# Optimization experiments

Measured on AMD Instinct MI355X. Metric: run time of the kernel, lower is better.

The kernel has to match this reference:

```python
import jax, jax.numpy as jnp
import numpy as np

N = 50000      # nodes
E = 800000     # edges (before self-loops)
G = 64         # graphs in batch
IN, HID, OUT, H = 128, 64, 64, 4
NEG_SLOPE = 0.2
BN_EPS = 1e-5


def setup_inputs() -> dict:
    key = jax.random.key(0)
    ks = jax.random.split(key, 16)
    s = 0.1
    return {
        "x": jax.random.normal(ks[0], (N, IN), jnp.float32),
        "edge_index": jax.random.randint(ks[1], (2, E), 0, N, dtype=jnp.int64),
        "batch": jnp.sort(jax.random.randint(ks[2], (N,), 0, G, dtype=jnp.int64)),
        "num_graphs": G,
        "W1": jax.random.normal(ks[3], (IN, H * HID), jnp.float32) * s,
        "att_src1": jax.random.normal(ks[4], (H, HID), jnp.float32) * s,
        "att_dst1": jax.random.normal(ks[5], (H, HID), jnp.float32) * s,
        "b1": jnp.zeros((HID,), jnp.float32),
        "W2": jax.random.normal(ks[6], (HID, H * OUT), jnp.float32) * s,
        "att_src2": jax.random.normal(ks[7], (H, OUT), jnp.float32) * s,
        "att_dst2": jax.random.normal(ks[8], (H, OUT), jnp.float32) * s,
        "b2": jnp.zeros((OUT,), jnp.float32),
        "gate_w1": jax.random.normal(ks[9], (OUT, OUT), jnp.float32) * s,
        "gate_b1": jnp.zeros((OUT,), jnp.float32),
        "bn_gamma": jnp.ones((OUT,), jnp.float32),
        "bn_beta": jnp.zeros((OUT,), jnp.float32),
        "gate_w2": jax.random.normal(ks[10], (OUT, 1), jnp.float32) * s,
        "gate_b2": jnp.zeros((1,), jnp.float32),
        "lin_w": jax.random.normal(ks[11], (OUT, 1), jnp.float32) * s,
        "lin_b": jnp.zeros((1,), jnp.float32),
    }


def segment_softmax(e, seg, num_segments):
    # numerically stable softmax over segments (per-destination / per-graph)
    m = jax.ops.segment_max(e, seg, num_segments=num_segments)
    m = jnp.where(jnp.isfinite(m), m, 0.0)
    ex = jnp.exp(e - m[seg])
    den = jax.ops.segment_sum(ex, seg, num_segments=num_segments)
    return ex / (den[seg] + 1e-16)


def gat_conv(x, src, dst, n, W, a_src, a_dst, b, heads, ch):
    h = (x @ W).reshape(n, heads, ch)                 # [N,H,C]
    asrc = jnp.sum(h * a_src, axis=-1)                # [N,H]
    adst = jnp.sum(h * a_dst, axis=-1)                # [N,H]
    e = jax.nn.leaky_relu(asrc[src] + adst[dst], NEG_SLOPE)   # [E',H]
    alpha = segment_softmax(e, dst, n)                # softmax over incoming edges
    out = jax.ops.segment_sum(h[src] * alpha[:, :, None], dst, num_segments=n)
    return jnp.mean(out, axis=1) + b                  # concat=False -> head mean


def reference(x, edge_index, batch, num_graphs, W1, att_src1, att_dst1, b1,
              W2, att_src2, att_dst2, b2, gate_w1, gate_b1, bn_gamma, bn_beta,
              gate_w2, gate_b2, lin_w, lin_b):
    n = x.shape[0]
    loop = jnp.arange(n, dtype=edge_index.dtype)      # PyG add_self_loops default
    src = jnp.concatenate([edge_index[0], loop])
    dst = jnp.concatenate([edge_index[1], loop])

    out = jax.nn.sigmoid(gat_conv(x, src, dst, n, W1, att_src1, att_dst1, b1, H, HID))
    out = jax.nn.sigmoid(gat_conv(out, src, dst, n, W2, att_src2, att_dst2, b2, H, OUT))

    # GlobalAttention pooling; gate_nn = Linear -> BN(eval, rm=0, rv=1) -> ReLU -> Linear
    g = out @ gate_w1 + gate_b1
    g = (g / jnp.sqrt(1.0 + BN_EPS)) * bn_gamma + bn_beta
    g = jax.nn.relu(g) @ gate_w2 + gate_b2            # [N,1]
    gate = segment_softmax(g, batch, num_graphs)      # per-graph softmax
    pooled = jax.ops.segment_sum(gate * out, batch, num_segments=num_graphs)  # [G,OUT]

    return jax.nn.sigmoid(pooled @ lin_w + lin_b)     # [G,1]
```

## Files before the change

kernel.cpp:

```cpp
#include <hip/hip_runtime.h>


constexpr int NN = 50000;
constexpr int EE = 800000;
constexpr int NG = 64;
constexpr float NEG = 0.2f;
constexpr int MT = NN / 16;
constexpr int SLOTS = 64;
constexpr int CH = 16;
constexpr int GB = (MT + 3) / 4;

constexpr int EB_EDGES = 4096;
constexpr int EBN = (EE + EB_EDGES - 1) / EB_EDGES;
constexpr int NBKT = (NN + 255) / 256;
constexpr int CAP = 48;
constexpr int OVFCAP = 8192;

static_assert(NN % 4 == 0, "aggregate barrier assumes no early-exit waves");

using bf16x8 = __attribute__((ext_vector_type(8))) __bf16;
using f32x4  = __attribute__((ext_vector_type(4))) float;
using f32x2  = __attribute__((ext_vector_type(2))) float;

__device__ __forceinline__ float wred(float v) {
#pragma unroll
  for (int o = 32; o; o >>= 1) v += __shfl_down(v, o);
  return v;
}
__device__ __forceinline__ float sigmoidf(float v) { return 1.f / (1.f + __expf(-v)); }
__device__ __forceinline__ float lrelu(float v) { return fmaxf(v, NEG * v); }
__device__ __forceinline__ unsigned short f2b(float f) {
  union { float f; unsigned u; } v; v.f = f;
  unsigned r = v.u + 0x7fff + ((v.u >> 16) & 1);
  return (unsigned short)(r >> 16);
}
__device__ __forceinline__ float b2f(unsigned short b) {
  union { unsigned u; float f; } v; v.u = ((unsigned)b) << 16;
  return v.f;
}

__global__ void prep_kernel(const float* __restrict__ W1, const float* __restrict__ W2,
                            const float* __restrict__ gw1, const float* __restrict__ gamma,
                            const int* __restrict__ batch,
                            unsigned short* __restrict__ W1b, unsigned short* __restrict__ W2b,
                            unsigned short* __restrict__ Bg, int* __restrict__ goffs,
                            int* __restrict__ ovf_cnt) {
  int b = blockIdx.x;
  if (b < 128) {
    int idx = b * 256 + threadIdx.x;
    int j = idx & 7, lane = (idx >> 3) & 63, rest = idx >> 9;
    int kc = rest & 3, ntile = rest >> 2;
    W1b[idx] = f2b(W1[(kc * 32 + (lane >> 4) * 8 + j) * 256 + ntile * 16 + (lane & 15)]);
    return;
  }
  if (b < 192) {
    int idx = (b - 128) * 256 + threadIdx.x;
    int j = idx & 7, lane = (idx >> 3) & 63, rest = idx >> 9;
    int kc = rest & 1, ntile = rest >> 1;
    W2b[idx] = f2b(W2[(kc * 32 + (lane >> 4) * 8 + j) * 256 + ntile * 16 + (lane & 15)]);
    return;
  }
  if (b < 208) {
    int idx = (b - 192) * 256 + threadIdx.x;
    int j = idx & 7, lane = (idx >> 3) & 63, rest = idx >> 9;
    int kc = rest & 1, nt = rest >> 1;
    int k = kc * 32 + (lane >> 4) * 8 + j;
    int n = nt * 16 + (lane & 15);
    Bg[idx] = f2b(gw1[k * 64 + n] * gamma[n] * rsqrtf(1.f + 1e-5f));
    return;
  }
  if (threadIdx.x == 0) *ovf_cnt = 0;
  int g = threadIdx.x;
  if (g <= NG) {
    int lo = 0, hi = NN;
    while (lo < hi) {
      int mid = (lo + hi) >> 1;
      if (batch[mid] < g) lo = mid + 1; else hi = mid;
    }
    goffs[g] = lo;
  }
}

template <int KC>
__device__ __forceinline__ void gemm_body(int mt, int lane, const bf16x8* av,
                                          const unsigned short* Bp,
                                          unsigned char* __restrict__ C8,
                                          const float* __restrict__ att_s,
                                          const float* __restrict__ att_d,
                                          float* __restrict__ asrc,
                                          float* __restrict__ adst) {
  int m0 = mt * 16;
  int q = lane >> 4, r = lane & 15;
  f32x4 acc[16] = {};
#pragma unroll
  for (int kc = 0; kc < KC; ++kc) {
#pragma unroll
    for (int nt = 0; nt < 16; ++nt) {
      bf16x8 b = *(const bf16x8*)&Bp[(((unsigned)nt * KC + kc) * 64 + lane) * 8];
      acc[nt] = __builtin_amdgcn_mfma_f32_16x16x32_bf16(av[kc], b, acc[nt], 0, 0, 0);
    }
  }
#pragma unroll
  for (int reg = 0; reg < 4; ++reg) {
    unsigned row = m0 + q * 4 + reg;
    uint4 pk;
    int w;
    w = __builtin_amdgcn_cvt_pk_fp8_f32(acc[0][reg], acc[1][reg], 0, false);
    w = __builtin_amdgcn_cvt_pk_fp8_f32(acc[2][reg], acc[3][reg], w, true);
    pk.x = (unsigned)w;
    w = __builtin_amdgcn_cvt_pk_fp8_f32(acc[4][reg], acc[5][reg], 0, false);
    w = __builtin_amdgcn_cvt_pk_fp8_f32(acc[6][reg], acc[7][reg], w, true);
    pk.y = (unsigned)w;
    w = __builtin_amdgcn_cvt_pk_fp8_f32(acc[8][reg], acc[9][reg], 0, false);
    w = __builtin_amdgcn_cvt_pk_fp8_f32(acc[10][reg], acc[11][reg], w, true);
    pk.z = (unsigned)w;
    w = __builtin_amdgcn_cvt_pk_fp8_f32(acc[12][reg], acc[13][reg], 0, false);
    w = __builtin_amdgcn_cvt_pk_fp8_f32(acc[14][reg], acc[15][reg], w, true);
    pk.w = (unsigned)w;
    *(uint4*)(C8 + (size_t)row * 256 + (unsigned)r * 16) = pk;
  }
  float ps[4][4] = {}, pd[4][4] = {};
#pragma unroll
  for (int head = 0; head < 4; ++head) {
#pragma unroll
    for (int i = 0; i < 4; ++i) {
      float sv = att_s[head * 64 + i * 16 + r];
      float dv = att_d[head * 64 + i * 16 + r];
#pragma unroll
      for (int reg = 0; reg < 4; ++reg) {
        ps[head][reg] += acc[head * 4 + i][reg] * sv;
        pd[head][reg] += acc[head * 4 + i][reg] * dv;
      }
    }
  }
#pragma unroll
  for (int head = 0; head < 4; ++head)
#pragma unroll
    for (int reg = 0; reg < 4; ++reg)
#pragma unroll
      for (int o = 1; o < 16; o <<= 1) {
        ps[head][reg] += __shfl_xor(ps[head][reg], o);
        pd[head][reg] += __shfl_xor(pd[head][reg], o);
      }
  if (r == 0) {
#pragma unroll
    for (int reg = 0; reg < 4; ++reg) {
      int row = m0 + q * 4 + reg;
#pragma unroll
      for (int head = 0; head < 4; ++head) {
        asrc[row * 4 + head] = ps[head][reg];
        adst[row * 4 + head] = pd[head][reg];
      }
    }
  }
}

__global__ void gemm1_build_kernel(const float* __restrict__ x,
                                   const unsigned short* __restrict__ W1b,
                                   unsigned char* __restrict__ C8,
                                   const float* __restrict__ att_s,
                                   const float* __restrict__ att_d,
                                   float* __restrict__ asrc, float* __restrict__ adst,
                                   const int* __restrict__ ei,
                                   unsigned* __restrict__ bins,
                                   int* __restrict__ binCnt,
                                   int* __restrict__ ovf_cnt,
                                   unsigned* __restrict__ ovf) {
  __shared__ union {
    unsigned short B[128 * 256];
    int hist[NBKT];
  } smem;
  int b = blockIdx.x;
  if (b < GB) {
    int wave = threadIdx.x >> 6, lane = threadIdx.x & 63;
    int mt0 = b * 4 + wave;
    int mt = min(mt0, MT - 1);
    int q = lane >> 4, r = lane & 15;
#pragma unroll
    for (int it = 0; it < 16; ++it)
      ((uint4*)smem.B)[it * 256 + threadIdx.x] = ((const uint4*)W1b)[it * 256 + threadIdx.x];
    bf16x8 av[4];
    {
      const float* Arow = x + (size_t)(mt * 16 + r) * 128 + q * 8;
      float4 f0[4], f1[4];
#pragma unroll
      for (int kc = 0; kc < 4; ++kc) {
        f0[kc] = *(const float4*)(Arow + kc * 32);
        f1[kc] = *(const float4*)(Arow + kc * 32 + 4);
      }
#pragma unroll
      for (int kc = 0; kc < 4; ++kc) {
        union { bf16x8 v; unsigned short s[8]; } u;
        u.s[0] = f2b(f0[kc].x); u.s[1] = f2b(f0[kc].y);
        u.s[2] = f2b(f0[kc].z); u.s[3] = f2b(f0[kc].w);
        u.s[4] = f2b(f1[kc].x); u.s[5] = f2b(f1[kc].y);
        u.s[6] = f2b(f1[kc].z); u.s[7] = f2b(f1[kc].w);
        av[kc] = u.v;
      }
    }
    __syncthreads();
    if (mt0 >= MT) return;
    gemm_body<4>(mt, lane, av, smem.B, C8, att_s, att_d, asrc, adst);
    return;
  }
  int hb = b - GB;
  for (int t = threadIdx.x; t < NBKT; t += 256) smem.hist[t] = 0;
  __syncthreads();
  int e0 = hb * EB_EDGES + threadIdx.x * 16;
#pragma unroll
  for (int k4 = 0; k4 < 4; ++k4) {
    int e = e0 + k4 * 4;
    if (e >= EE) break;
    int4 s4 = *(const int4*)&ei[e];
    int4 d4 = *(const int4*)&ei[EE + e];
    int ss[4] = {s4.x, s4.y, s4.z, s4.w};
    int dd[4] = {d4.x, d4.y, d4.z, d4.w};
#pragma unroll
    for (int u = 0; u < 4; ++u) {
      if (e + u >= EE) break;
      int src = ss[u], dst = dd[u];
      int bkt = dst >> 8;
      int rr = atomicAdd(&smem.hist[bkt], 1);
      if (rr < CAP) {
        bins[((unsigned)hb * NBKT + bkt) * CAP + rr] =
            (unsigned)src | ((unsigned)(dst & 255) << 16);
      } else {
        int o = atomicAdd(ovf_cnt, 1);
        if (o < OVFCAP) ovf[o] = (unsigned)src | ((unsigned)dst << 16);
      }
    }
  }
  __syncthreads();
  for (int t = threadIdx.x; t < NBKT; t += 256) binCnt[hb * NBKT + t] = smem.hist[t];
}

__global__ __launch_bounds__(1024) void csr_build_kernel(
    const unsigned* __restrict__ bins, const int* __restrict__ binCnt,
    const int* __restrict__ ovf_cnt, const unsigned* __restrict__ ovf,
    unsigned short* __restrict__ csr16, int* __restrict__ cnt) {
  int b = blockIdx.x;
  __shared__ int hist[256];
  int t = threadIdx.x;
  int node0 = b << 8;
  if (t < 256) {
    hist[t] = 1;
    int node = node0 + t;
    if (node < NN) csr16[(unsigned)node * SLOTS] = (unsigned short)node;
  }
  __syncthreads();
  int wave = t >> 6, lane = t & 63;
  for (int i = wave; i < EBN; i += 16) {
    int c = binCnt[i * NBKT + b];
    if (c > CAP) c = CAP;
    for (int base = 0; base < c; base += 64) {
      int j = base + lane;
      if (j < c) {
        unsigned p = bins[((unsigned)i * NBKT + b) * CAP + j];
        int dl = p >> 16, src = p & 0xffff;
        int r = atomicAdd(&hist[dl], 1);
        if (r < SLOTS) csr16[(unsigned)(node0 + dl) * SLOTS + r] = (unsigned short)src;
      }
    }
  }
  __syncthreads();
  int oc = *ovf_cnt;
  if (oc > OVFCAP) oc = OVFCAP;
  for (int j = t; j < oc; j += 1024) {
    unsigned p = ovf[j];
    int dst = (int)(p >> 16);
    if ((dst >> 8) == b) {
      int r = atomicAdd(&hist[dst & 255], 1);
      if (r < SLOTS) csr16[(unsigned)dst * SLOTS + r] = (unsigned short)(p & 0xffff);
    }
  }
  __syncthreads();
  if (t < 256) {
    int node = node0 + t;
    if (node < NN) cnt[node] = hist[t];
  }
}

__global__ void aggregate_kernel(const unsigned char* __restrict__ h8,
                                 const float* __restrict__ asrc,
                                 const float* __restrict__ adst,
                                 const int* __restrict__ cnt,
                                 const unsigned short* __restrict__ csr_src,
                                 const float* __restrict__ bias,
                                 unsigned short* __restrict__ outb) {
  int wave = threadIdx.x >> 6, lane = threadIdx.x & 63;
  int node = blockIdx.x * 4 + wave;
  int deg = min(cnt[node], SLOTS);
  int hgrp = lane >> 4;
  int q4 = lane >> 4;
  int r16 = lane & 15;
  float adh = adst[node * 4 + hgrp];
  int src_all = csr_src[(unsigned)node * SLOTS + lane];
  __shared__ float wtab[4][256];
  float* wlds = wtab[wave];
  float den = 0.f;
#pragma unroll
  for (int i = 0; i < 4; ++i) {
    int slot = i * 16 + r16;
    float w = 0.f;
    if (i * 16 < deg) {
      int s = __shfl(src_all, slot);
      bool valid = slot < deg;
      float xv = asrc[(unsigned)(valid ? s : 0) * 4 + hgrp];
      w = valid ? __expf(lrelu(xv + adh)) : 0.f;
    }
    wlds[slot * 4 + hgrp] = w;
    den += w;
  }
#pragma unroll
  for (int o = 1; o < 16; o <<= 1) den += __shfl_xor(den, o);

  const unsigned char* hp = h8 + (unsigned)r16 * 16;
  f32x2 a[8] = {};
#define ACC4(d, wA, wB, wC, wD)                                              \
  {                                                                          \
    a[0] += __builtin_amdgcn_cvt_pk_f32_fp8((d).x, false) * (wA);            \
    a[1] += __builtin_amdgcn_cvt_pk_f32_fp8((d).x, true) * (wA);             \
    a[2] += __builtin_amdgcn_cvt_pk_f32_fp8((d).y, false) * (wB);            \
    a[3] += __builtin_amdgcn_cvt_pk_f32_fp8((d).y, true) * (wB);             \
    a[4] += __builtin_amdgcn_cvt_pk_f32_fp8((d).z, false) * (wC);            \
    a[5] += __builtin_amdgcn_cvt_pk_f32_fp8((d).z, true) * (wC);             \
    a[6] += __builtin_amdgcn_cvt_pk_f32_fp8((d).w, false) * (wD);            \
    a[7] += __builtin_amdgcn_cvt_pk_f32_fp8((d).w, true) * (wD);             \
  }
  int e = 0;
#pragma unroll
  for (int i = 0; i < 4; ++i) {
    if (e >= deg) break;
    int bound = min(deg, (i + 1) * 16);
    if (bound - e == 16) {
      int eq = e + q4;
      int s0 = __shfl(src_all, eq);
      int s1 = __shfl(src_all, eq + 4);
      int s2 = __shfl(src_all, eq + 8);
      int s3 = __shfl(src_all, eq + 12);
      f32x4 w0 = *(const f32x4*)&wlds[(unsigned)eq * 4];
      f32x4 w1 = *(const f32x4*)&wlds[(unsigned)(eq + 4) * 4];
      f32x4 w2 = *(const f32x4*)&wlds[(unsigned)(eq + 8) * 4];
      f32x4 w3 = *(const f32x4*)&wlds[(unsigned)(eq + 12) * 4];
      uint4 d0 = *(const uint4*)(hp + ((unsigned)s0 << 8));
      uint4 d1 = *(const uint4*)(hp + ((unsigned)s1 << 8));
      uint4 d2 = *(const uint4*)(hp + ((unsigned)s2 << 8));
      uint4 d3 = *(const uint4*)(hp + ((unsigned)s3 << 8));
      ACC4(d0, w0[0], w0[1], w0[2], w0[3]);
      ACC4(d1, w1[0], w1[1], w1[2], w1[3]);
      ACC4(d2, w2[0], w2[1], w2[2], w2[3]);
      ACC4(d3, w3[0], w3[1], w3[2], w3[3]);
      e += 16;
    } else {
      for (; e < bound; e += 4) {
        int gg = min(4, bound - e);
        int q4e = min(q4, gg - 1);
        int su = __shfl(src_all, e + q4e);
        f32x4 wv = *(const f32x4*)&wlds[(unsigned)(e + q4e) * 4];
        if (q4 >= gg) { wv[0] = 0.f; wv[1] = 0.f; wv[2] = 0.f; wv[3] = 0.f; }
        uint4 d = *(const uint4*)(hp + ((unsigned)su << 8));
        ACC4(d, wv[0], wv[1], wv[2], wv[3]);
      }
    }
  }
#undef ACC4
  float dh0 = __shfl(den, 0), dh1 = __shfl(den, 16);
  float dh2 = __shfl(den, 32), dh3 = __shfl(den, 48);
  float i0 = 0.25f / (dh0 + 1e-16f), i1 = 0.25f / (dh1 + 1e-16f);
  float i2 = 0.25f / (dh2 + 1e-16f), i3 = 0.25f / (dh3 + 1e-16f);
  f32x4 v0 = {a[0].x * i0, a[0].y * i0, a[1].x * i0, a[1].y * i0};
  f32x4 v1 = {a[2].x * i1, a[2].y * i1, a[3].x * i1, a[3].y * i1};
  f32x4 v2 = {a[4].x * i2, a[4].y * i2, a[5].x * i2, a[5].y * i2};
  f32x4 v3 = {a[6].x * i3, a[6].y * i3, a[7].x * i3, a[7].y * i3};
  __shared__ float red[4][1056];
  float* wb2 = &red[wave][(unsigned)lane * 16 + (lane & 7) * 4];
  *(f32x4*)(wb2 + 0) = v0;
  *(f32x4*)(wb2 + 4) = v1;
  *(f32x4*)(wb2 + 8) = v2;
  *(f32x4*)(wb2 + 12) = v3;
  __syncthreads();
  const float* rb = &red[wave][0];
  int base = (lane & 15) * 16 + (lane & 7) * 4 + (lane >> 4);
  float s = 0.f;
#pragma unroll
  for (int q = 0; q < 4; ++q)
#pragma unroll
    for (int h = 0; h < 4; ++h)
      s += rb[q * 256 + base + 4 * h];
  float ov = sigmoidf(s + bias[lane]);
  outb[(size_t)node * 64 + lane] = f2b(ov);
}

__global__ void gemm2_kernel(const unsigned short* __restrict__ out1b,
                             const unsigned short* __restrict__ W2b,
                             unsigned char* __restrict__ C8,
                             const float* __restrict__ att_s,
                             const float* __restrict__ att_d,
                             float* __restrict__ asrc, float* __restrict__ adst) {
  __shared__ unsigned short B2[64 * 256];
  int wave = threadIdx.x >> 6, lane = threadIdx.x & 63;
  int mt0 = blockIdx.x * 4 + wave;
  int mt = min(mt0, MT - 1);
  int q = lane >> 4, r = lane & 15;
#pragma unroll
  for (int it = 0; it < 8; ++it)
    ((uint4*)B2)[it * 256 + threadIdx.x] = ((const uint4*)W2b)[it * 256 + threadIdx.x];
  bf16x8 av[2];
  {
    const unsigned short* Ar = out1b + (size_t)(mt * 16 + r) * 64 + q * 8;
    av[0] = *(const bf16x8*)(Ar);
    av[1] = *(const bf16x8*)(Ar + 32);
  }
  __syncthreads();
  if (mt0 >= MT) return;
  gemm_body<2>(mt, lane, av, B2, C8, att_s, att_d, asrc, adst);
}

__global__ void pool_partial_kernel(const int* __restrict__ goffs,
                                    const unsigned short* __restrict__ out2b,
                                    const unsigned short* __restrict__ Bg,
                                    const float* __restrict__ gb1,
                                    const float* __restrict__ gamma,
                                    const float* __restrict__ beta,
                                    const float* __restrict__ gw2,
                                    const float* __restrict__ gb2,
                                    float* __restrict__ part_acc,
                                    float* __restrict__ part_den) {
  int b = blockIdx.x, j = blockIdx.y;
  int beg = goffs[b], end = goffs[b + 1];
  int chunk = (end - beg + CH - 1) / CH;
  int cb = beg + j * chunk;
  int ce = min(end, cb + chunk);
  int lane = threadIdx.x & 63, wave = threadIdx.x >> 6;
  int q = lane >> 4, r = lane & 15;
  const float s = rsqrtf(1.f + 1e-5f);
  float gb2v = gb2[0];
  float accv = 0.f, den = 0.f;
  for (int n0 = cb + wave * 16; n0 < ce; n0 += 64) {
    f32x4 acc[4] = {};
    int row = n0 + r;
    if (row >= NN) row = NN - 1;
    const unsigned short* Arow = out2b + (size_t)row * 64 + q * 8;
#pragma unroll
    for (int kc = 0; kc < 2; ++kc) {
      bf16x8 a = *(const bf16x8*)(Arow + kc * 32);
#pragma unroll
      for (int nt = 0; nt < 4; ++nt) {
        bf16x8 b8 = *(const bf16x8*)&Bg[(((size_t)nt * 2 + kc) * 64 + lane) * 8];
        acc[nt] = __builtin_amdgcn_mfma_f32_16x16x32_bf16(a, b8, acc[nt], 0, 0, 0);
      }
    }
    float sum[4] = {0.f, 0.f, 0.f, 0.f};
#pragma unroll
    for (int nt = 0; nt < 4; ++nt) {
      int col = nt * 16 + r;
      float off = gb1[col] * gamma[col] * s + beta[col];
      float w2 = gw2[col];
#pragma unroll
      for (int reg = 0; reg < 4; ++reg)
        sum[reg] += fmaxf(acc[nt][reg] + off, 0.f) * w2;
    }
#pragma unroll
    for (int reg = 0; reg < 4; ++reg)
#pragma unroll
      for (int o = 1; o < 16; o <<= 1) sum[reg] += __shfl_xor(sum[reg], o);
    float gx[4];
#pragma unroll
    for (int reg = 0; reg < 4; ++reg) {
      int n = n0 + q * 4 + reg;
      gx[reg] = (n < ce) ? __expf(sum[reg] + gb2v) : 0.f;
    }
#pragma unroll
    for (int t = 0; t < 16; ++t) {
      int n = n0 + t;
      if (n >= ce) break;
      float gv = __shfl(gx[t & 3], (t >> 2) << 4);
      accv += gv * b2f(out2b[(size_t)n * 64 + lane]);
      den += gv;
    }
  }
  __shared__ float sacc[4][64];
  __shared__ float sden[4];
  sacc[wave][lane] = accv;
  if (lane == 0) sden[wave] = den;
  __syncthreads();
  if (wave == 0) {
    float a = sacc[0][lane] + sacc[1][lane] + sacc[2][lane] + sacc[3][lane];
    part_acc[((size_t)b * CH + j) * 64 + lane] = a;
    if (lane == 0) part_den[b * CH + j] = sden[0] + sden[1] + sden[2] + sden[3];
  }
}

__global__ void pool_final_kernel(const float* __restrict__ part_acc,
                                  const float* __restrict__ part_den,
                                  const float* __restrict__ lw, const float* __restrict__ lb,
                                  float* __restrict__ out) {
  int b = blockIdx.x, lane = threadIdx.x;
  float a = 0.f;
#pragma unroll
  for (int j = 0; j < CH; ++j) a += part_acc[((size_t)b * CH + j) * 64 + lane];
  float den = (lane < CH) ? part_den[b * CH + lane] : 0.f;
  den = wred(den);
  den = __shfl(den, 0);
  float p = a / (den + 1e-16f);
  float v = wred(p * lw[lane]);
  if (lane == 0) out[b] = sigmoidf(v + lb[0]);
}

extern "C" void kernel_launch(void* const* d_in, const int* in_sizes, int n_in,
                              void* d_out, int out_size, void* d_ws, size_t ws_size,
                              hipStream_t stream) {
  const float* x    = (const float*)d_in[0];
  const int*   ei   = (const int*)d_in[1];
  const int*   batch= (const int*)d_in[2];
  const float* W1   = (const float*)d_in[4];
  const float* as1  = (const float*)d_in[5];
  const float* ad1  = (const float*)d_in[6];
  const float* b1   = (const float*)d_in[7];
  const float* W2   = (const float*)d_in[8];
  const float* as2  = (const float*)d_in[9];
  const float* ad2  = (const float*)d_in[10];
  const float* b2   = (const float*)d_in[11];
  const float* gw1  = (const float*)d_in[12];
  const float* gb1  = (const float*)d_in[13];
  const float* gamma= (const float*)d_in[14];
  const float* beta = (const float*)d_in[15];
  const float* gw2  = (const float*)d_in[16];
  const float* gb2  = (const float*)d_in[17];
  const float* lw   = (const float*)d_in[18];
  const float* lb   = (const float*)d_in[19];
  float* out = (float*)d_out;

  char* ws = (char*)d_ws;
  size_t off = 0;
  auto alloc = [&](size_t bytes) -> void* {
    void* p = ws + off;
    off = (off + bytes + 255) & ~(size_t)255;
    return p;
  };
  unsigned short* W1b    = (unsigned short*)alloc((size_t)128 * 256 * 2);
  unsigned short* W2b    = (unsigned short*)alloc((size_t)64 * 256 * 2);
  unsigned short* Bg     = (unsigned short*)alloc((size_t)64 * 64 * 2);
  unsigned char*  h8     = (unsigned char*)alloc((size_t)NN * 256);
  unsigned short* out1b  = (unsigned short*)alloc((size_t)NN * 64 * 2);
  unsigned short* out2b  = (unsigned short*)alloc((size_t)NN * 64 * 2);
  float*    asrc    = (float*)alloc((size_t)NN * 4 * 4);
  float*    adst    = (float*)alloc((size_t)NN * 4 * 4);
  int*      cnt     = (int*)alloc((size_t)NN * 4);
  unsigned short* csr16 = (unsigned short*)alloc((size_t)NN * SLOTS * 2);
  unsigned* bins    = (unsigned*)alloc((size_t)EBN * NBKT * CAP * 4);
  int*      binCnt  = (int*)alloc((size_t)EBN * NBKT * 4);
  int*      ovf_cnt = (int*)alloc(256);
  unsigned* ovf     = (unsigned*)alloc((size_t)OVFCAP * 4);
  int*      goffs   = (int*)alloc((size_t)(NG + 1) * 4);
  float*    pacc    = (float*)alloc((size_t)NG * CH * 64 * 4);
  float*    pden    = (float*)alloc((size_t)NG * CH * 4);

  const int nodeBlocks = NN / 4;

  prep_kernel<<<209, 256, 0, stream>>>(W1, W2, gw1, gamma, batch,
                                       W1b, W2b, Bg, goffs, ovf_cnt);

  gemm1_build_kernel<<<GB + EBN, 256, 0, stream>>>(x, W1b, h8, as1, ad1, asrc, adst,
                                                   ei, bins, binCnt, ovf_cnt, ovf);
  csr_build_kernel<<<NBKT, 1024, 0, stream>>>(bins, binCnt, ovf_cnt, ovf, csr16, cnt);

  aggregate_kernel<<<nodeBlocks, 256, 0, stream>>>(h8, asrc, adst, cnt, csr16, b1, out1b);

  gemm2_kernel<<<GB, 256, 0, stream>>>(out1b, W2b, h8, as2, ad2, asrc, adst);
  aggregate_kernel<<<nodeBlocks, 256, 0, stream>>>(h8, asrc, adst, cnt, csr16, b2, out2b);

  pool_partial_kernel<<<dim3(NG, CH), 256, 0, stream>>>(goffs, out2b, Bg, gb1, gamma, beta,
                                                        gw2, gb2, pacc, pden);
  pool_final_kernel<<<NG, 64, 0, stream>>>(pacc, pden, lw, lb, out);
}
```

Before: 242.4 us.

## Fuse layer-1 aggregation with layer-2 GEMM into one kernel

Merges the first aggregation and the second GEMM into a single kernel. Each block aggregates 16 nodes into an LDS tile and runs MFMA on it directly, so the out1b round trip through global memory and one launch go away. The aggregation helper now uses wave barriers instead of block-wide syncs. Layer 2 writes to separate h8b/asrc2/adst2 buffers, which avoids overwriting data other blocks are still reading. In exchange, each block serialises four nodes per wave before the GEMM, which lowers parallelism within the aggregation and may expose gather latency.

```diff
diff --git a/kernel.cpp b/kernel.cpp
--- a/kernel.cpp
+++ b/kernel.cpp
@@ -16,7 +16,7 @@
 constexpr int CAP = 48;
 constexpr int OVFCAP = 8192;
 
-static_assert(NN % 4 == 0, "aggregate barrier assumes no early-exit waves");
+static_assert(NN % 16 == 0, "fused block = 16 nodes");
 
 using bf16x8 = __attribute__((ext_vector_type(8))) __bf16;
 using f32x4  = __attribute__((ext_vector_type(4))) float;
@@ -280,23 +280,18 @@
   }
 }
 
-__global__ void aggregate_kernel(const unsigned char* __restrict__ h8,
-                                 const float* __restrict__ asrc,
-                                 const float* __restrict__ adst,
-                                 const int* __restrict__ cnt,
-                                 const unsigned short* __restrict__ csr_src,
-                                 const float* __restrict__ bias,
-                                 unsigned short* __restrict__ outb) {
-  int wave = threadIdx.x >> 6, lane = threadIdx.x & 63;
-  int node = blockIdx.x * 4 + wave;
+__device__ __forceinline__ float agg_node(int node, int lane,
+                                          float* __restrict__ wlds,
+                                          float* __restrict__ redw,
+                                          const unsigned char* __restrict__ h8,
+                                          const float* __restrict__ asrc,
+                                          const float* __restrict__ adst,
+                                          const int* __restrict__ cnt,
+                                          const unsigned short* __restrict__ csr_src) {
+  int q4 = lane >> 4, r16 = lane & 15, hgrp = q4;
   int deg = min(cnt[node], SLOTS);
-  int hgrp = lane >> 4;
-  int q4 = lane >> 4;
-  int r16 = lane & 15;
   float adh = adst[node * 4 + hgrp];
   int src_all = csr_src[(unsigned)node * SLOTS + lane];
-  __shared__ float wtab[4][256];
-  float* wlds = wtab[wave];
   float den = 0.f;
 #pragma unroll
   for (int i = 0; i < 4; ++i) {
@@ -313,6 +308,7 @@
   }
 #pragma unroll
   for (int o = 1; o < 16; o <<= 1) den += __shfl_xor(den, o);
+  __builtin_amdgcn_wave_barrier();
 
   const unsigned char* hp = h8 + (unsigned)r16 * 16;
   f32x2 a[8] = {};
@@ -372,48 +368,110 @@
   f32x4 v1 = {a[2].x * i1, a[2].y * i1, a[3].x * i1, a[3].y * i1};
   f32x4 v2 = {a[4].x * i2, a[4].y * i2, a[5].x * i2, a[5].y * i2};
   f32x4 v3 = {a[6].x * i3, a[6].y * i3, a[7].x * i3, a[7].y * i3};
-  __shared__ float red[4][1056];
-  float* wb2 = &red[wave][(unsigned)lane * 16 + (lane & 7) * 4];
+  float* wb2 = &redw[(unsigned)lane * 16 + (lane & 7) * 4];
   *(f32x4*)(wb2 + 0) = v0;
   *(f32x4*)(wb2 + 4) = v1;
   *(f32x4*)(wb2 + 8) = v2;
   *(f32x4*)(wb2 + 12) = v3;
-  __syncthreads();
-  const float* rb = &red[wave][0];
+  __builtin_amdgcn_wave_barrier();
   int base = (lane & 15) * 16 + (lane & 7) * 4 + (lane >> 4);
   float s = 0.f;
 #pragma unroll
   for (int q = 0; q < 4; ++q)
 #pragma unroll
     for (int h = 0; h < 4; ++h)
-      s += rb[q * 256 + base + 4 * h];
+      s += redw[q * 256 + base + 4 * h];
+  return s;
+}
+
+__global__ void agg1_gemm2_kernel(const unsigned char* __restrict__ h8,
+                                  const float* __restrict__ asrc1,
+                                  const float* __restrict__ adst1,
+                                  const int* __restrict__ cnt,
+                                  const unsigned short* __restrict__ csr_src,
+                                  const float* __restrict__ b1,
+                                  const unsigned short* __restrict__ W2b,
+                                  const float* __restrict__ as2,
+                                  const float* __restrict__ ad2,
+                                  unsigned char* __restrict__ h8b,
+                                  float* __restrict__ asrc2,
+                                  float* __restrict__ adst2) {
+  int wv = threadIdx.x >> 6, lane = threadIdx.x & 63;
+  __shared__ float wtab[4][256];
+  __shared__ union { float red[4][1056]; unsigned ctile[16 * 64]; } sm;
+  __shared__ unsigned short A16[16][72];
+  for (int nl = 0; nl < 4; ++nl) {
+    int rl = wv * 4 + nl;
+    int node = blockIdx.x * 16 + rl;
+    float s = agg_node(node, lane, wtab[wv], sm.red[wv], h8, asrc1, adst1, cnt, csr_src);
+    A16[rl][lane] = f2b(sigmoidf(s + b1[lane]));
+  }
+  __syncthreads();
+  int q = lane >> 4, r = lane & 15;
+  bf16x8 a0 = *(const bf16x8*)&A16[r][q * 8];
+  bf16x8 a1 = *(const bf16x8*)&A16[r][q * 8 + 32];
+  f32x4 acc[4] = {};
+#pragma unroll
+  for (int ntl = 0; ntl < 4; ++ntl) {
+    int ntg = wv * 4 + ntl;
+    bf16x8 b0 = *(const bf16x8*)&W2b[(((unsigned)ntg * 2 + 0) * 64 + lane) * 8];
+    bf16x8 bq = *(const bf16x8*)&W2b[(((unsigned)ntg * 2 + 1) * 64 + lane) * 8];
+    acc[ntl] = __builtin_amdgcn_mfma_f32_16x16x32_bf16(a0, b0, acc[ntl], 0, 0, 0);
+    acc[ntl] = __builtin_amdgcn_mfma_f32_16x16x32_bf16(a1, bq, acc[ntl], 0, 0, 0);
+  }
+  float ps[4] = {}, pd[4] = {};
+#pragma unroll
+  for (int i = 0; i < 4; ++i) {
+    float sv = as2[wv * 64 + i * 16 + r];
+    float dv = ad2[wv * 64 + i * 16 + r];
+#pragma unroll
+    for (int reg = 0; reg < 4; ++reg) {
+      ps[reg] += acc[i][reg] * sv;
+      pd[reg] += acc[i][reg] * dv;
+    }
+  }
+#pragma unroll
+  for (int reg = 0; reg < 4; ++reg)
+#pragma unroll
+    for (int o = 1; o < 16; o <<= 1) {
+      ps[reg] += __shfl_xor(ps[reg], o);
+      pd[reg] += __shfl_xor(pd[reg], o);
+    }
+  if (r == 0) {
+#pragma unroll
+    for (int reg = 0; reg < 4; ++reg) {
+      int row = blockIdx.x * 16 + q * 4 + reg;
+      asrc2[row * 4 + wv] = ps[reg];
+      adst2[row * 4 + wv] = pd[reg];
+    }
+  }
+#pragma unroll
+  for (int reg = 0; reg < 4; ++reg) {
+    int rowl = q * 4 + reg;
+    int w = __builtin_amdgcn_cvt_pk_fp8_f32(acc[0][reg], acc[1][reg], 0, false);
+    w = __builtin_amdgcn_cvt_pk_fp8_f32(acc[2][reg], acc[3][reg], w, true);
+    sm.ctile[rowl * 64 + r * 4 + wv] = (unsigned)w;
+  }
+  __syncthreads();
+  int row = threadIdx.x >> 4, seg = threadIdx.x & 15;
+  uint4 v = *(const uint4*)&sm.ctile[row * 64 + seg * 4];
+  *(uint4*)(h8b + ((size_t)(blockIdx.x * 16 + row)) * 256 + (unsigned)seg * 16) = v;
+}
+
+__global__ void aggregate_kernel(const unsigned char* __restrict__ h8,
+                                 const float* __restrict__ asrc,
+                                 const float* __restrict__ adst,
+                                 const int* __restrict__ cnt,
+                                 const unsigned short* __restrict__ csr_src,
+                                 const float* __restrict__ bias,
+                                 unsigned short* __restrict__ outb) {
+  int wave = threadIdx.x >> 6, lane = threadIdx.x & 63;
+  int node = blockIdx.x * 4 + wave;
+  __shared__ float wtab[4][256];
+  __shared__ float red[4][1056];
+  float s = agg_node(node, lane, wtab[wave], red[wave], h8, asrc, adst, cnt, csr_src);
   float ov = sigmoidf(s + bias[lane]);
   outb[(size_t)node * 64 + lane] = f2b(ov);
-}
-
-__global__ void gemm2_kernel(const unsigned short* __restrict__ out1b,
-                             const unsigned short* __restrict__ W2b,
-                             unsigned char* __restrict__ C8,
-                             const float* __restrict__ att_s,
-                             const float* __restrict__ att_d,
-                             float* __restrict__ asrc, float* __restrict__ adst) {
-  __shared__ unsigned short B2[64 * 256];
-  int wave = threadIdx.x >> 6, lane = threadIdx.x & 63;
-  int mt0 = blockIdx.x * 4 + wave;
-  int mt = min(mt0, MT - 1);
-  int q = lane >> 4, r = lane & 15;
-#pragma unroll
-  for (int it = 0; it < 8; ++it)
-    ((uint4*)B2)[it * 256 + threadIdx.x] = ((const uint4*)W2b)[it * 256 + threadIdx.x];
-  bf16x8 av[2];
-  {
-    const unsigned short* Ar = out1b + (size_t)(mt * 16 + r) * 64 + q * 8;
-    av[0] = *(const bf16x8*)(Ar);
-    av[1] = *(const bf16x8*)(Ar + 32);
-  }
-  __syncthreads();
-  if (mt0 >= MT) return;
-  gemm_body<2>(mt, lane, av, B2, C8, att_s, att_d, asrc, adst);
 }
 
 __global__ void pool_partial_kernel(const int* __restrict__ goffs,
@@ -542,10 +600,12 @@
   unsigned short* W2b    = (unsigned short*)alloc((size_t)64 * 256 * 2);
   unsigned short* Bg     = (unsigned short*)alloc((size_t)64 * 64 * 2);
   unsigned char*  h8     = (unsigned char*)alloc((size_t)NN * 256);
-  unsigned short* out1b  = (unsigned short*)alloc((size_t)NN * 64 * 2);
+  unsigned char*  h8b    = (unsigned char*)alloc((size_t)NN * 256);
   unsigned short* out2b  = (unsigned short*)alloc((size_t)NN * 64 * 2);
   float*    asrc    = (float*)alloc((size_t)NN * 4 * 4);
   float*    adst    = (float*)alloc((size_t)NN * 4 * 4);
+  float*    asrc2   = (float*)alloc((size_t)NN * 4 * 4);
+  float*    adst2   = (float*)alloc((size_t)NN * 4 * 4);
   int*      cnt     = (int*)alloc((size_t)NN * 4);
   unsigned short* csr16 = (unsigned short*)alloc((size_t)NN * SLOTS * 2);
   unsigned* bins    = (unsigned*)alloc((size_t)EBN * NBKT * CAP * 4);
@@ -556,8 +616,6 @@
   float*    pacc    = (float*)alloc((size_t)NG * CH * 64 * 4);
   float*    pden    = (float*)alloc((size_t)NG * CH * 4);
 
-  const int nodeBlocks = NN / 4;
-
   prep_kernel<<<209, 256, 0, stream>>>(W1, W2, gw1, gamma, batch,
                                        W1b, W2b, Bg, goffs, ovf_cnt);
 
@@ -565,10 +623,10 @@
                                                    ei, bins, binCnt, ovf_cnt, ovf);
   csr_build_kernel<<<NBKT, 1024, 0, stream>>>(bins, binCnt, ovf_cnt, ovf, csr16, cnt);
 
-  aggregate_kernel<<<nodeBlocks, 256, 0, stream>>>(h8, asrc, adst, cnt, csr16, b1, out1b);
-
-  gemm2_kernel<<<GB, 256, 0, stream>>>(out1b, W2b, h8, as2, ad2, asrc, adst);
-  aggregate_kernel<<<nodeBlocks, 256, 0, stream>>>(h8, asrc, adst, cnt, csr16, b2, out2b);
+  agg1_gemm2_kernel<<<MT, 256, 0, stream>>>(h8, asrc, adst, cnt, csr16, b1,
+                                            W2b, as2, ad2, h8b, asrc2, adst2);
+
+  aggregate_kernel<<<NN / 4, 256, 0, stream>>>(h8b, asrc2, adst2, cnt, csr16, b2, out2b);
 
   pool_partial_kernel<<<dim3(NG, CH), 256, 0, stream>>>(goffs, out2b, Bg, gb1, gamma, beta,
                                                         gw2, gb2, pacc, pden);
```

Measured after the change: 239.0 us. No clear change (-1.4%).
